# Performance work log

Hardware: AMD Instinct MI355X
Metric: run time of the kernel (lower is better)

## Reference

```python
import jax, jax.numpy as jnp
import numpy as np

N = 12288   # num_nodes
D = 128     # isize
K_TOP = 31  # k + 1, per top_k(similarities, self.k + 1)


def setup_inputs() -> dict:
    key = jax.random.key(0)
    features = jax.random.normal(key, (N, D), dtype=jnp.float32)
    eye = jnp.eye(D, dtype=jnp.float32)  # param_init: weight <- I, bias <- 0
    return {
        "features": features,
        "W1": eye,
        "b1": jnp.zeros((D,), jnp.float32),
        "W2": eye,
        "b2": jnp.zeros((D,), jnp.float32),
    }


def reference(features, W1, b1, W2, b2):
    # internal_forward: Linear -> ReLU -> Linear (nlayers=2, act='relu')
    h = jax.nn.relu(features @ W1.T + b1)
    h = h @ W2.T + b2
    # F.normalize(h, dim=1, p=2) with eps=1e-12
    hn = h / jnp.maximum(jnp.linalg.norm(h, axis=1, keepdims=True), 1e-12)
    # dense N x N cosine similarity
    sim = hn @ hn.T
    # top_k: keep top (k+1) entries per row, zero elsewhere; then apply_non_linearity='relu'
    vals, idx = jax.lax.top_k(sim, K_TOP)          # [N, K_TOP]
    rows = jnp.arange(sim.shape[0])[:, None]       # [N, 1]
    # relu(sim * mask) == scatter relu(top-k values) into a zero matrix
    out = jnp.zeros_like(sim).at[rows, idx].set(jax.nn.relu(vals))
    return out
```

## Files before the change

### kernel.cpp

```cpp
#include <hip/hip_runtime.h>
#include <stdint.h>
#include <math.h>

#define NN 12288
#define DD 128
#define KTOP 31
#define TCAND 64
#define CCAP 128
#define RPB 16
#define WPB 8
#define LDEP 14
#define NSTREAM 32
#define KPR (NSTREAM * LDEP)
#define KPL (KPR / 64)
#define ITERS 48

typedef __attribute__((ext_vector_type(8))) short bf16x8;
typedef __attribute__((ext_vector_type(4))) float f32x4;

__device__ __forceinline__ unsigned short f2bf(float x) {
  unsigned int u = __float_as_uint(x);
  u += 0x7fffu + ((u >> 16) & 1u);
  return (unsigned short)(u >> 16);
}

__device__ __forceinline__ unsigned umed3(unsigned a, unsigned b, unsigned c) {
  unsigned d;
  asm("v_med3_u32 %0, %1, %2, %3" : "=v"(d) : "v"(a), "v"(b), "v"(c));
  return d;
}

#define PINS(P) { \
  const unsigned p_ = (P); \
  _Pragma("unroll") \
  for (int i_ = 0; i_ < LDEP - 1; ++i_) \
    L[i_] = umed3(p_, L[i_], L[i_ + 1]); \
  L[LDEP - 1] = L[LDEP - 1] > p_ ? L[LDEP - 1] : p_; }

__global__ __launch_bounds__(128)
void wtrans_kernel(const float* __restrict__ W1, const float* __restrict__ W2,
                   float* __restrict__ W1T, float* __restrict__ W2T) {
  const int r = blockIdx.x, c = threadIdx.x;
  W1T[(size_t)c * DD + r] = W1[(size_t)r * DD + c];
  W2T[(size_t)c * DD + r] = W2[(size_t)r * DD + c];
}

__global__ __launch_bounds__(128)
void mlp_norm_kernel(const float* __restrict__ feat,
                     const float* __restrict__ W1T, const float* __restrict__ b1,
                     const float* __restrict__ W2T, const float* __restrict__ b2,
                     double* __restrict__ hn64, unsigned short* __restrict__ hnb) {
  __shared__ double bufA[8][DD];
  __shared__ double bufB[8][DD];
  __shared__ double mnorm[8];
  const int t = threadIdx.x;
  const int row0 = blockIdx.x * 8;

  #pragma unroll
  for (int rr = 0; rr < 8; ++rr)
    bufA[rr][t] = (double)feat[(size_t)(row0 + rr) * DD + t];
  __syncthreads();

  {
    double acc[8] = {0,0,0,0,0,0,0,0};
    for (int k = 0; k < DD; k += 2) {
      double w0 = (double)W1T[(size_t)k * DD + t];
      double w1 = (double)W1T[(size_t)(k + 1) * DD + t];
      #pragma unroll
      for (int rr = 0; rr < 8; ++rr) {
        double2 a2 = *(const double2*)(&bufA[rr][k]);
        acc[rr] = fma(w0, a2.x, acc[rr]);
        acc[rr] = fma(w1, a2.y, acc[rr]);
      }
    }
    double bb = (double)b1[t];
    #pragma unroll
    for (int rr = 0; rr < 8; ++rr)
      bufB[rr][t] = fmax(acc[rr] + bb, 0.0);
  }
  __syncthreads();
  {
    double acc[8] = {0,0,0,0,0,0,0,0};
    for (int k = 0; k < DD; k += 2) {
      double w0 = (double)W2T[(size_t)k * DD + t];
      double w1 = (double)W2T[(size_t)(k + 1) * DD + t];
      #pragma unroll
      for (int rr = 0; rr < 8; ++rr) {
        double2 a2 = *(const double2*)(&bufB[rr][k]);
        acc[rr] = fma(w0, a2.x, acc[rr]);
        acc[rr] = fma(w1, a2.y, acc[rr]);
      }
    }
    double bb = (double)b2[t];
    #pragma unroll
    for (int rr = 0; rr < 8; ++rr)
      bufA[rr][t] = acc[rr] + bb;
  }
  __syncthreads();

  const int lane = t & 63;
  const int w = t >> 6;
  #pragma unroll
  for (int r2 = 0; r2 < 4; ++r2) {
    int rr = w * 4 + r2;
    double x0 = bufA[rr][lane];
    double x1 = bufA[rr][lane + 64];
    double s = x0 * x0 + x1 * x1;
    #pragma unroll
    for (int d = 1; d < 64; d <<= 1)
      s += __shfl_xor(s, d);
    if (lane == 0) mnorm[rr] = fmax(sqrt(s), 1e-12);
  }
  __syncthreads();
  #pragma unroll
  for (int rr = 0; rr < 8; ++rr) {
    double v = bufA[rr][t] / mnorm[rr];
    hn64[(size_t)(row0 + rr) * DD + t] = v;
    hnb[(size_t)(row0 + rr) * DD + t] = f2bf((float)v);
  }
}

__global__ __launch_bounds__(512, 6)
void fused_kernel(const unsigned short* __restrict__ hnb,
                  const double* __restrict__ hn64,
                  float* __restrict__ out) {
  __shared__ unsigned keybuf[RPB][KPR + 1];
  __shared__ unsigned scand[WPB][CCAP];
  __shared__ double cres[WPB][CCAP];
  __shared__ float outv[RPB][KTOP];
  __shared__ int   outc[RPB][KTOP];
  const int t = threadIdx.x, lane = t & 63, wv = t >> 6;
  const int m = lane & 15, quad = lane >> 4;
  const int row0 = blockIdx.x * RPB;

  bf16x8 afrag[4];
  #pragma unroll
  for (int kc = 0; kc < 4; ++kc)
    afrag[kc] = *(const bf16x8*)(hnb + (size_t)(row0 + m) * DD + kc * 32 + quad * 8);

  unsigned L[LDEP];
  #pragma unroll
  for (int i = 0; i < LDEP; ++i) L[i] = 0;

  f32x4* outz = (f32x4*)(out + (size_t)(row0 + wv * 2) * NN);
  const f32x4 z = {0.0f, 0.0f, 0.0f, 0.0f};

  for (int it = 0; it < ITERS; ++it) {
    const int cb = it * (WPB * 32) + wv * 32;
    f32x4 acc0 = {0.0f, 0.0f, 0.0f, 0.0f};
    f32x4 acc1 = {0.0f, 0.0f, 0.0f, 0.0f};
    #pragma unroll
    for (int kc = 0; kc < 4; ++kc) {
      bf16x8 b0 = *(const bf16x8*)(hnb + (size_t)(cb + m) * DD + kc * 32 + quad * 8);
      bf16x8 b1 = *(const bf16x8*)(hnb + (size_t)(cb + 16 + m) * DD + kc * 32 + quad * 8);
      acc0 = __builtin_amdgcn_mfma_f32_16x16x32_bf16(b0, afrag[kc], acc0, 0, 0, 0);
      acc1 = __builtin_amdgcn_mfma_f32_16x16x32_bf16(b1, afrag[kc], acc1, 0, 0, 0);
    }
    __builtin_nontemporal_store(z, &outz[it * 128 + lane]);
    __builtin_nontemporal_store(z, &outz[it * 128 + 64 + lane]);
    #pragma unroll
    for (int r = 0; r < 4; ++r) {
      {
        unsigned bf = f2bf(acc0[r]);
        unsigned s = (bf & 0x8000u) ? 0u : bf;
        unsigned p = (s << 16) | (unsigned)(cb + quad * 4 + r);
        PINS(p)
      }
      {
        unsigned bf = f2bf(acc1[r]);
        unsigned s = (bf & 0x8000u) ? 0u : bf;
        unsigned p = (s << 16) | (unsigned)(cb + 16 + quad * 4 + r);
        PINS(p)
      }
    }
  }

  #pragma unroll
  for (int d = 0; d < LDEP; ++d)
    keybuf[m][(wv * 4 + quad) * LDEP + d] = L[d];
  __syncthreads();

  for (int ii = 0; ii < 2; ++ii) {
    const int lr = wv * 2 + ii;
    const int grow = row0 + lr;
    unsigned k7[KPL];
    #pragma unroll
    for (int i = 0; i < KPL; ++i)
      k7[i] = keybuf[lr][lane * KPL + i];

    unsigned lo = 0, hi = 0xFFFFu;
    while (lo < hi) {
      unsigned mid = (lo + hi + 1) >> 1;
      int c = 0;
      #pragma unroll
      for (int i = 0; i < KPL; ++i) c += (int)((k7[i] >> 16) >= mid);
      #pragma unroll
      for (int d = 1; d < 64; d <<= 1) c += __shfl_xor(c, d);
      if (c >= TCAND) lo = mid; else hi = mid - 1;
    }
    const unsigned thr = lo;

    int cl = 0;
    #pragma unroll
    for (int i = 0; i < KPL; ++i) cl += (int)((k7[i] >> 16) >= thr);
    int pre = cl;
    #pragma unroll
    for (int d = 1; d < 64; d <<= 1) {
      int y = __shfl_up(pre, d);
      if (lane >= d) pre += y;
    }
    const int total = __shfl(pre, 63);
    const int nc = total < CCAP ? total : CCAP;
    int slot = pre - cl;
    #pragma unroll
    for (int i = 0; i < KPL; ++i) {
      if ((k7[i] >> 16) >= thr) {
        if (slot < CCAP) scand[wv][slot] = k7[i];
        ++slot;
      }
    }

    const double* arow = hn64 + (size_t)grow * DD;
    const int hl = lane >> 5;
    const int kl = (lane & 31) * 4;
    const double a0 = arow[kl], a1 = arow[kl + 1], a2 = arow[kl + 2], a3 = arow[kl + 3];
    const int ng = (nc + 1) >> 1;
    for (int g = 0; g < ng; ++g) {
      const int ci = 2 * g + hl;
      double partial = 0.0;
      if (ci < nc) {
        const int col = (int)(scand[wv][ci] & 0xFFFFu);
        const double* brow = hn64 + (size_t)col * DD + kl;
        double2 b01 = *(const double2*)(brow);
        double2 b23 = *(const double2*)(brow + 2);
        partial = fma(a0, b01.x, fma(a1, b01.y, fma(a2, b23.x, a3 * b23.y)));
      }
      #pragma unroll
      for (int d = 1; d < 32; d <<= 1)
        partial += __shfl_xor(partial, d);
      if ((lane & 31) == 0 && ci < nc) cres[wv][ci] = partial;
    }
    double rv0 = -1.0e300, rv1 = -1.0e300;
    int rc0 = 0x7fffffff, rc1 = 0x7fffffff;
    if (lane < nc)      { rv0 = cres[wv][lane];      rc0 = (int)(scand[wv][lane] & 0xFFFFu); }
    if (lane + 64 < nc) { rv1 = cres[wv][lane + 64]; rc1 = (int)(scand[wv][lane + 64] & 0xFFFFu); }

    for (int itk = 0; itk < KTOP; ++itk) {
      bool f = (rv0 > rv1) || (rv0 == rv1 && rc0 < rc1);
      double bv = f ? rv0 : rv1;
      int bc = f ? rc0 : rc1;
      #pragma unroll
      for (int d = 1; d < 64; d <<= 1) {
        double ov = __shfl_xor(bv, d);
        int    oc = __shfl_xor(bc, d);
        bool tk = (ov > bv) || (ov == bv && oc < bc);
        bv = tk ? ov : bv;
        bc = tk ? oc : bc;
      }
      if (lane == itk) {
        outv[lr][itk] = (float)fmax(bv, 0.0);
        outc[lr][itk] = bc;
      }
      if (rv0 == bv && rc0 == bc) rv0 = -1.0e300;
      else if (rv1 == bv && rc1 == bc) rv1 = -1.0e300;
    }
  }

  asm volatile("s_waitcnt vmcnt(0)" ::: "memory");
  #pragma unroll
  for (int ii = 0; ii < 2; ++ii) {
    const int lr = wv * 2 + ii;
    if (lane < KTOP)
      out[(size_t)(row0 + lr) * NN + outc[lr][lane]] = outv[lr][lane];
  }
}

extern "C" void kernel_launch(void* const* d_in, const int* in_sizes, int n_in,
                              void* d_out, int out_size, void* d_ws, size_t ws_size,
                              hipStream_t stream) {
  const float* feat = (const float*)d_in[0];
  const float* W1 = (const float*)d_in[1];
  const float* b1 = (const float*)d_in[2];
  const float* W2 = (const float*)d_in[3];
  const float* b2 = (const float*)d_in[4];
  float* out = (float*)d_out;

  double* hn64 = (double*)d_ws;
  unsigned short* hnb = (unsigned short*)(hn64 + (size_t)NN * DD);
  float* W1T = (float*)(hnb + (size_t)NN * DD);
  float* W2T = W1T + DD * DD;

  wtrans_kernel<<<DD, DD, 0, stream>>>(W1, W2, W1T, W2T);
  mlp_norm_kernel<<<NN / 8, 128, 0, stream>>>(feat, W1T, b1, W2T, b2, hn64, hnb);
  fused_kernel<<<NN / RPB, 512, 0, stream>>>(hnb, hn64, out);
}
```

Baseline: 947.0 us.

## Split zero-fill and scatter out of similarity kernel into separate emit kernel

The zeroing of the dense N×N output and the scatter of the top-k values move out of the similarity/selection kernel into a new emit kernel. The selection kernel now writes per-row values and column indices to a workspace buffer. The intent is to free the MFMA and selection loop from the large streaming stores that were interleaved with it. The cost is that the ~600 MB zero-fill no longer overlaps with compute and becomes its own bandwidth-bound pass. The MLP/normalize kernel also doubles its block to 256 threads, with each block now handling 16 rows.

```diff
diff --git a/kernel.cpp b/kernel.cpp
--- a/kernel.cpp
+++ b/kernel.cpp
@@ -45,56 +45,58 @@
   W2T[(size_t)c * DD + r] = W2[(size_t)r * DD + c];
 }
 
-__global__ __launch_bounds__(128)
+__global__ __launch_bounds__(256)
 void mlp_norm_kernel(const float* __restrict__ feat,
                      const float* __restrict__ W1T, const float* __restrict__ b1,
                      const float* __restrict__ W2T, const float* __restrict__ b2,
                      double* __restrict__ hn64, unsigned short* __restrict__ hnb) {
-  __shared__ double bufA[8][DD];
-  __shared__ double bufB[8][DD];
-  __shared__ double mnorm[8];
+  __shared__ double bufA[16][DD];
+  __shared__ double bufB[16][DD];
+  __shared__ double mnorm[16];
   const int t = threadIdx.x;
-  const int row0 = blockIdx.x * 8;
+  const int c = t & 127;
+  const int g = t >> 7;
+  const int row0 = blockIdx.x * 16 + g * 8;
 
   #pragma unroll
   for (int rr = 0; rr < 8; ++rr)
-    bufA[rr][t] = (double)feat[(size_t)(row0 + rr) * DD + t];
+    bufA[g * 8 + rr][c] = (double)feat[(size_t)(row0 + rr) * DD + c];
   __syncthreads();
 
   {
     double acc[8] = {0,0,0,0,0,0,0,0};
     for (int k = 0; k < DD; k += 2) {
-      double w0 = (double)W1T[(size_t)k * DD + t];
-      double w1 = (double)W1T[(size_t)(k + 1) * DD + t];
+      double w0 = (double)W1T[(size_t)k * DD + c];
+      double w1 = (double)W1T[(size_t)(k + 1) * DD + c];
       #pragma unroll
       for (int rr = 0; rr < 8; ++rr) {
-        double2 a2 = *(const double2*)(&bufA[rr][k]);
+        double2 a2 = *(const double2*)(&bufA[g * 8 + rr][k]);
         acc[rr] = fma(w0, a2.x, acc[rr]);
         acc[rr] = fma(w1, a2.y, acc[rr]);
       }
     }
-    double bb = (double)b1[t];
+    double bb = (double)b1[c];
     #pragma unroll
     for (int rr = 0; rr < 8; ++rr)
-      bufB[rr][t] = fmax(acc[rr] + bb, 0.0);
+      bufB[g * 8 + rr][c] = fmax(acc[rr] + bb, 0.0);
   }
   __syncthreads();
   {
     double acc[8] = {0,0,0,0,0,0,0,0};
     for (int k = 0; k < DD; k += 2) {
-      double w0 = (double)W2T[(size_t)k * DD + t];
-      double w1 = (double)W2T[(size_t)(k + 1) * DD + t];
+      double w0 = (double)W2T[(size_t)k * DD + c];
+      double w1 = (double)W2T[(size_t)(k + 1) * DD + c];
       #pragma unroll
       for (int rr = 0; rr < 8; ++rr) {
-        double2 a2 = *(const double2*)(&bufB[rr][k]);
+        double2 a2 = *(const double2*)(&bufB[g * 8 + rr][k]);
         acc[rr] = fma(w0, a2.x, acc[rr]);
         acc[rr] = fma(w1, a2.y, acc[rr]);
       }
     }
-    double bb = (double)b2[t];
+    double bb = (double)b2[c];
     #pragma unroll
     for (int rr = 0; rr < 8; ++rr)
-      bufA[rr][t] = acc[rr] + bb;
+      bufA[g * 8 + rr][c] = acc[rr] + bb;
   }
   __syncthreads();
 
@@ -114,21 +116,19 @@
   __syncthreads();
   #pragma unroll
   for (int rr = 0; rr < 8; ++rr) {
-    double v = bufA[rr][t] / mnorm[rr];
-    hn64[(size_t)(row0 + rr) * DD + t] = v;
-    hnb[(size_t)(row0 + rr) * DD + t] = f2bf((float)v);
+    double v = bufA[g * 8 + rr][c] / mnorm[g * 8 + rr];
+    hn64[(size_t)(row0 + rr) * DD + c] = v;
+    hnb[(size_t)(row0 + rr) * DD + c] = f2bf((float)v);
   }
 }
 
 __global__ __launch_bounds__(512, 6)
-void fused_kernel(const unsigned short* __restrict__ hnb,
-                  const double* __restrict__ hn64,
-                  float* __restrict__ out) {
+void simsel_kernel(const unsigned short* __restrict__ hnb,
+                   const double* __restrict__ hn64,
+                   float* __restrict__ resval, int* __restrict__ rescol) {
   __shared__ unsigned keybuf[RPB][KPR + 1];
   __shared__ unsigned scand[WPB][CCAP];
   __shared__ double cres[WPB][CCAP];
-  __shared__ float outv[RPB][KTOP];
-  __shared__ int   outc[RPB][KTOP];
   const int t = threadIdx.x, lane = t & 63, wv = t >> 6;
   const int m = lane & 15, quad = lane >> 4;
   const int row0 = blockIdx.x * RPB;
@@ -141,9 +141,6 @@
   unsigned L[LDEP];
   #pragma unroll
   for (int i = 0; i < LDEP; ++i) L[i] = 0;
-
-  f32x4* outz = (f32x4*)(out + (size_t)(row0 + wv * 2) * NN);
-  const f32x4 z = {0.0f, 0.0f, 0.0f, 0.0f};
 
   for (int it = 0; it < ITERS; ++it) {
     const int cb = it * (WPB * 32) + wv * 32;
@@ -156,8 +153,6 @@
       acc0 = __builtin_amdgcn_mfma_f32_16x16x32_bf16(b0, afrag[kc], acc0, 0, 0, 0);
       acc1 = __builtin_amdgcn_mfma_f32_16x16x32_bf16(b1, afrag[kc], acc1, 0, 0, 0);
     }
-    __builtin_nontemporal_store(z, &outz[it * 128 + lane]);
-    __builtin_nontemporal_store(z, &outz[it * 128 + 64 + lane]);
     #pragma unroll
     for (int r = 0; r < 4; ++r) {
       {
@@ -258,21 +253,31 @@
         bc = tk ? oc : bc;
       }
       if (lane == itk) {
-        outv[lr][itk] = (float)fmax(bv, 0.0);
-        outc[lr][itk] = bc;
+        resval[(size_t)grow * KTOP + itk] = (float)fmax(bv, 0.0);
+        rescol[(size_t)grow * KTOP + itk] = bc;
       }
       if (rv0 == bv && rc0 == bc) rv0 = -1.0e300;
       else if (rv1 == bv && rc1 == bc) rv1 = -1.0e300;
     }
   }
-
-  asm volatile("s_waitcnt vmcnt(0)" ::: "memory");
-  #pragma unroll
-  for (int ii = 0; ii < 2; ++ii) {
-    const int lr = wv * 2 + ii;
-    if (lane < KTOP)
-      out[(size_t)(row0 + lr) * NN + outc[lr][lane]] = outv[lr][lane];
-  }
+}
+
+__global__ __launch_bounds__(256)
+void emit_kernel(const float* __restrict__ resval, const int* __restrict__ rescol,
+                 float* __restrict__ out) {
+  const int row = blockIdx.x, t = threadIdx.x;
+  float v = 0.0f; int c = 0;
+  if (t < KTOP) {
+    v = resval[(size_t)row * KTOP + t];
+    c = rescol[(size_t)row * KTOP + t];
+  }
+  f32x4* orow = (f32x4*)(out + (size_t)row * NN);
+  const f32x4 z = {0.0f, 0.0f, 0.0f, 0.0f};
+  #pragma unroll
+  for (int i = 0; i < NN / 4 / 256; ++i)
+    __builtin_nontemporal_store(z, &orow[i * 256 + t]);
+  __syncthreads();
+  if (t < KTOP) out[(size_t)row * NN + c] = v;
 }
 
 extern "C" void kernel_launch(void* const* d_in, const int* in_sizes, int n_in,
@@ -287,10 +292,13 @@
 
   double* hn64 = (double*)d_ws;
   unsigned short* hnb = (unsigned short*)(hn64 + (size_t)NN * DD);
-  float* W1T = (float*)(hnb + (size_t)NN * DD);
+  float* resval = (float*)(hnb + (size_t)NN * DD);
+  int* rescol = (int*)(resval + (size_t)NN * KTOP);
+  float* W1T = (float*)(rescol + (size_t)NN * KTOP);
   float* W2T = W1T + DD * DD;
 
   wtrans_kernel<<<DD, DD, 0, stream>>>(W1, W2, W1T, W2T);
-  mlp_norm_kernel<<<NN / 8, 128, 0, stream>>>(feat, W1T, b1, W2T, b2, hn64, hnb);
-  fused_kernel<<<NN / RPB, 512, 0, stream>>>(hnb, hn64, out);
-}
+  mlp_norm_kernel<<<NN / 16, 256, 0, stream>>>(feat, W1T, b1, W2T, b2, hn64, hnb);
+  simsel_kernel<<<NN / RPB, 512, 0, stream>>>(hnb, hn64, resval, rescol);
+  emit_kernel<<<NN, 256, 0, stream>>>(resval, rescol, out);
+}
```

Result: slower. 1.066 ms (+12.6%).
